# Kernel tuning notes

Hardware: AMD Instinct MI355X
Metric: run time of the kernel (lower is better)

Reference implementation:

```python
import jax, jax.numpy as jnp
import numpy as np

B, T, D = 16, 2048, 1024


def setup_inputs() -> dict:
    key = jax.random.key(0)
    ks = jax.random.split(key, 7)
    s = 1.0 / np.sqrt(D)  # nn.Linear default init bound
    u = lambda k, shape: jax.random.uniform(k, shape, jnp.float32, -s, s)
    return {
        "x": jax.random.normal(ks[0], (B, T, D), jnp.float32),
        "h0": jnp.zeros((B, D), jnp.float32),
        "W_in": u(ks[1], (2 * D, D)),
        "b_in": u(ks[2], (2 * D,)),
        "W_dt": u(ks[3], (D, D)),
        "b_dt": u(ks[4], (D,)),
        "W_out": u(ks[5], (D, D)),
        "b_out": u(ks[6], (D,)),
    }


def reference(x, h0, W_in, b_in, W_dt, b_dt, W_out, b_out):
    # in_proj then chunk: first half x_part, second half gate
    xz = jnp.einsum("btd,ed->bte", x, W_in) + b_in          # [B,T,2D]
    x_part, gate = jnp.split(xz, 2, axis=-1)                  # each [B,T,D]
    dt = jax.nn.sigmoid(jnp.einsum("btd,ed->bte", x_part, W_dt) + b_dt)  # [B,T,D]

    def step(h, inp):
        dt_t, xp_t = inp                                      # [B,D] each
        h = (1.0 - dt_t) * h + dt_t * xp_t                    # gated EMA update
        return h, h

    _, hs = jax.lax.scan(step, h0,
                         (jnp.swapaxes(dt, 0, 1), jnp.swapaxes(x_part, 0, 1)))
    hs = jnp.swapaxes(hs, 0, 1)                               # [B,T,D]
    y = jnp.einsum("btd,ed->bte", hs * jax.nn.sigmoid(gate), W_out) + b_out
    return y
```

## Files before the change

kernel.cpp:

```cpp
#include <hip/hip_runtime.h>
#include <hip/hip_bf16.h>
#include <cstdint>

typedef __attribute__((ext_vector_type(8))) short short8;
typedef __attribute__((ext_vector_type(4))) float f32x4;
typedef __attribute__((ext_vector_type(8))) unsigned short ushort8;

#define B_ 16
#define T_ 2048
#define D_ 1024
#define M_ (B_*T_)
#define NC 32
#define CL 64

static __device__ __forceinline__ float bf2f(unsigned short u) {
  unsigned int x = ((unsigned int)u) << 16;
  return __builtin_bit_cast(float, x);
}
static __device__ __forceinline__ unsigned short f2bf(float f) {
  unsigned int x = __builtin_bit_cast(unsigned int, f);
  unsigned int r = x + 0x7fffu + ((x >> 16) & 1u);
  return (unsigned short)(r >> 16);
}
static __device__ __forceinline__ float sigmoidf(float v) {
  return 1.f / (1.f + __expf(-v));
}

typedef const __attribute__((address_space(1))) unsigned int* gas1_t;
typedef __attribute__((address_space(3))) unsigned int* las3_t;
static __device__ __forceinline__ void async_copy16(const void* g, void* l) {
  __builtin_amdgcn_global_load_lds((gas1_t)g, (las3_t)l, 16, 0, 0);
}

#define VMCNT4 asm volatile("s_waitcnt vmcnt(4)" ::: "memory")
#define VMCNT2 asm volatile("s_waitcnt vmcnt(2)" ::: "memory")
#define VMCNT0 asm volatile("s_waitcnt vmcnt(0)" ::: "memory")
#define LGKM0  asm volatile("s_waitcnt lgkmcnt(0)" ::: "memory")
#define SBAR   __builtin_amdgcn_s_barrier()
#define SCHED0 __builtin_amdgcn_sched_barrier(0)

__global__ void cvt_all(const float* __restrict__ x,  unsigned short* __restrict__ xb,
                        const float* __restrict__ w1, unsigned short* __restrict__ o1,
                        const float* __restrict__ w2, unsigned short* __restrict__ o2,
                        const float* __restrict__ w3, unsigned short* __restrict__ o3) {
  long i = (long)blockIdx.x * blockDim.x + threadIdx.x;
  long stride = (long)gridDim.x * blockDim.x;
  for (; i < 4718592; i += stride) {
    const float* src; unsigned short* dst; long off;
    if (i < 4194304)      { src = x;  dst = xb; off = i; }
    else if (i < 4456448) { src = w1; dst = o1; off = i - 4194304; }
    else if (i < 4587520) { src = w2; dst = o2; off = i - 4456448; }
    else                  { src = w3; dst = o3; off = i - 4587520; }
    const float4* p = (const float4*)(src + off * 8);
    float4 a = p[0], b = p[1];
    ushort8 o;
    o[0] = f2bf(a.x); o[1] = f2bf(a.y); o[2] = f2bf(a.z); o[3] = f2bf(a.w);
    o[4] = f2bf(b.x); o[5] = f2bf(b.y); o[6] = f2bf(b.z); o[7] = f2bf(b.w);
    *(ushort8*)(dst + off * 8) = o;
  }
}

template<int EPI>
__global__ __launch_bounds__(512, 2) void gemm256(
    const unsigned short* __restrict__ A, long lda,
    const unsigned short* __restrict__ Bw,
    const float* __restrict__ bias,
    void* __restrict__ Cout, long ldc,
    int nbx)
{
  constexpr int KT = 16;
  __shared__ __align__(16) unsigned short lds[65536];

  const int tid = threadIdx.x;
  const int l  = tid & 63, w = tid >> 6;
  const int wm = w >> 2, wn = w & 3;
  const int fr = l & 15, g = l >> 4;
  const int t8 = tid >> 3;
  const int c8x = ((l & 7) ^ (l >> 3)) << 4;
  const int s0 = ((g ^ (fr & 7)) << 4);
  const int aoff  = wm * 8192 + fr * 128 + s0;
  const int aoff1 = aoff ^ 0x40;
  const int boff  = 65536 + wn * 4096 + fr * 128 + s0;
  const int boff1 = boff ^ 0x40;
  const int tB = (w >> 2) * 64 + (w & 3) * 8 + (l >> 3);

  const int nwg = gridDim.x;
  const int cpx = nwg >> 3;
  const int bid = blockIdx.x;
  const int swz = (bid & 7) * cpx + (bid >> 3);
  const long m0 = (long)(swz / nbx) * 256;
  const long n0 = (long)(swz % nbx) * 256;

  const char* Ab = (const char*)A;
  const char* Bb = (const char*)Bw;
  const long ldab = lda * 2;
  char* LB = (char*)lds;

  auto stA = [&](int kt, int h, int nb) {
    char* lb = LB + nb * 32768 + h * 16384 + w * 1024;
    long col = (long)kt * 128 + c8x;
    async_copy16(Ab + (m0 + h * 64 + t8) * ldab + col, lb);
    async_copy16(Ab + (m0 + 128 + h * 64 + t8) * ldab + col, lb + 8192);
  };
  auto stB = [&](int kt, int h, int nb) {
    char* lb = LB + 65536 + nb * 32768 + h * 16384 + w * 1024;
    long col = (long)kt * 128 + c8x;
    async_copy16(Bb + (n0 + tB + h * 32) * 2048 + col, lb);
    async_copy16(Bb + (n0 + tB + 128 + h * 32) * 2048 + col, lb + 8192);
  };

  f32x4 acc[8][4] = {};
  short8 af0[4][2], af1[4][2], bf0[2][2], bf1[2][2];

#define RD_A(DST, MH, CUR) do {                                                \
    const char* p0_ = LB + (CUR) * 32768 + (MH) * 16384 + aoff;                \
    const char* p1_ = LB + (CUR) * 32768 + (MH) * 16384 + aoff1;               \
    _Pragma("unroll") for (int mi = 0; mi < 4; ++mi) {                         \
      DST[mi][0] = *(const short8*)(p0_ + mi * 2048);                          \
      DST[mi][1] = *(const short8*)(p1_ + mi * 2048); }                        \
  } while (0)
#define RD_B(DST, NH, CUR) do {                                                \
    const char* p0_ = LB + (CUR) * 32768 + (NH) * 16384 + boff;                \
    const char* p1_ = LB + (CUR) * 32768 + (NH) * 16384 + boff1;               \
    _Pragma("unroll") for (int ni = 0; ni < 2; ++ni) {                         \
      DST[ni][0] = *(const short8*)(p0_ + ni * 2048);                          \
      DST[ni][1] = *(const short8*)(p1_ + ni * 2048); }                        \
  } while (0)
#define MM(AF, BF, MB, NB) do {                                                \
    __builtin_amdgcn_s_setprio(1);                                             \
    _Pragma("unroll") for (int mi = 0; mi < 4; ++mi)                           \
    _Pragma("unroll") for (int ni = 0; ni < 2; ++ni) {                         \
      acc[(MB)+mi][(NB)+ni] = __builtin_amdgcn_mfma_f32_16x16x32_bf16(         \
          AF[mi][0], BF[ni][0], acc[(MB)+mi][(NB)+ni], 0, 0, 0);               \
      acc[(MB)+mi][(NB)+ni] = __builtin_amdgcn_mfma_f32_16x16x32_bf16(         \
          AF[mi][1], BF[ni][1], acc[(MB)+mi][(NB)+ni], 0, 0, 0); }             \
    __builtin_amdgcn_s_setprio(0);                                             \
  } while (0)

  stA(0, 0, 0); stB(0, 0, 0); stA(0, 1, 0); stB(0, 1, 0);
  VMCNT0; SCHED0; SBAR;
  RD_A(af0, 0, 0); RD_B(bf0, 0, 0); SCHED0;

  for (int t = 0; t < KT; ++t) {
    const int cur = t & 1, nxt = cur ^ 1;
    const bool nl = (t + 1 < KT);
    RD_A(af1, 1, cur); SCHED0;
    if (nl) { stA(t + 1, 0, nxt); stB(t + 1, 0, nxt); } SCHED0;
    MM(af0, bf0, 0, 0);
    if (nl) { VMCNT4; } else { VMCNT0; }
    SCHED0; SBAR; SCHED0;
    RD_B(bf1, 1, cur); SCHED0;
    if (nl) { stA(t + 1, 1, nxt); stB(t + 1, 1, nxt); } SCHED0;
    MM(af1, bf0, 4, 0);
    SCHED0; SBAR; SCHED0;
    MM(af1, bf1, 4, 2);
    if (nl) { VMCNT4; }
    SCHED0; SBAR; SCHED0;
    MM(af0, bf1, 0, 2);
    SCHED0;
    if (nl) { RD_A(af0, 0, nxt); RD_B(bf0, 0, nxt); }
    SCHED0;
    if (nl) { VMCNT2; }
    SCHED0; SBAR; SCHED0;
  }
#undef RD_A
#undef RD_B
#undef MM

  __syncthreads();

  char* ep = LB + w * 16384;
  const int rq = l >> 4;
  if (EPI != 2) {
#pragma unroll
    for (int mi = 0; mi < 8; ++mi)
#pragma unroll
      for (int ni = 0; ni < 4; ++ni) {
        int cl = ni * 16 + fr;
        float bv = bias[n0 + wn * 64 + cl];
#pragma unroll
        for (int r = 0; r < 4; ++r) {
          float v = acc[mi][ni][r] + bv;
          if (EPI == 1) v = sigmoidf(v);
          int row = mi * 16 + rq * 4 + r;
          int byte = (row * 128 + cl * 2) ^ ((row & 7) << 4);
          *(unsigned short*)(ep + byte) = f2bf(v);
        }
      }
    LGKM0; SCHED0;
#pragma unroll
    for (int i = 0; i < 16; ++i) {
      int row = i * 8 + (l >> 3);
      int cb = (l & 7) * 16;
      int byte = (row * 128 + cb) ^ ((row & 7) << 4);
      short8 v = *(const short8*)(ep + byte);
      *(short8*)((unsigned short*)Cout + (m0 + wm * 128 + row) * ldc
                 + n0 + wn * 64 + (cb >> 1)) = v;
    }
  } else {
#pragma unroll
    for (int p = 0; p < 2; ++p) {
#pragma unroll
      for (int mi = 0; mi < 4; ++mi)
#pragma unroll
        for (int ni = 0; ni < 4; ++ni) {
          int cl = ni * 16 + fr;
          float bv = bias[n0 + wn * 64 + cl];
#pragma unroll
          for (int r = 0; r < 4; ++r) {
            float v = acc[p * 4 + mi][ni][r] + bv;
            int row = mi * 16 + rq * 4 + r;
            int byte = (row * 256 + cl * 4) ^ ((row & 7) << 4);
            *(float*)(ep + byte) = v;
          }
        }
      LGKM0; SCHED0;
#pragma unroll
      for (int i = 0; i < 16; ++i) {
        int row = i * 4 + (l >> 4);
        int cb = (l & 15) * 16;
        int byte = (row * 256 + cb) ^ ((row & 7) << 4);
        f32x4 v = *(const f32x4*)(ep + byte);
        *(f32x4*)((float*)Cout + (m0 + wm * 128 + p * 64 + row) * ldc
                  + n0 + wn * 64 + (cb >> 2)) = v;
      }
      LGKM0; SCHED0;
    }
  }
}

__global__ void scan_passA(const unsigned short* __restrict__ dtb,
                           const unsigned short* __restrict__ xz,
                           float* __restrict__ P, float* __restrict__ Hl)
{
  int idx = blockIdx.x * blockDim.x + threadIdx.x;
  int d8 = idx & 127;
  int c  = (idx >> 7) & 31;
  int b  = idx >> 12;
  int d0 = d8 * 8;
  long mbase = (long)b * T_ + (long)c * CL;
  float h[8] = {0,0,0,0,0,0,0,0};
  float p[8] = {1,1,1,1,1,1,1,1};
  for (int t = 0; t < CL; ++t) {
    long m = mbase + t;
    ushort8 dv = *(const ushort8*)(dtb + m * D_ + d0);
    ushort8 xv = *(const ushort8*)(xz + m * (2 * D_) + d0);
#pragma unroll
    for (int j = 0; j < 8; ++j) {
      float dt = bf2f(dv[j]);
      float xp = bf2f(xv[j]);
      float om = 1.f - dt;
      h[j] = om * h[j] + dt * xp;
      p[j] *= om;
    }
  }
  long pb = ((long)(b * NC + c)) * D_ + d0;
#pragma unroll
  for (int j = 0; j < 8; ++j) { P[pb + j] = p[j]; Hl[pb + j] = h[j]; }
}

__global__ void scan_passC(unsigned short* dts,
                           const unsigned short* __restrict__ xz,
                           const float* __restrict__ h0,
                           const float* __restrict__ P,
                           const float* __restrict__ Hl)
{
  int idx = blockIdx.x * blockDim.x + threadIdx.x;
  int d8 = idx & 127;
  int c  = (idx >> 7) & 31;
  int b  = idx >> 12;
  int d0 = d8 * 8;
  long mbase = (long)b * T_ + (long)c * CL;

  float h[8];
#pragma unroll
  for (int j = 0; j < 8; ++j) h[j] = h0[(long)b * D_ + d0 + j];

  for (int jc = 0; jc < c; ++jc) {
    long pb = ((long)(b * NC + jc)) * D_ + d0;
    float pj[8], hj[8];
    *(f32x4*)&pj[0] = *(const f32x4*)(P + pb);
    *(f32x4*)&pj[4] = *(const f32x4*)(P + pb + 4);
    *(f32x4*)&hj[0] = *(const f32x4*)(Hl + pb);
    *(f32x4*)&hj[4] = *(const f32x4*)(Hl + pb + 4);
#pragma unroll
    for (int j = 0; j < 8; ++j) h[j] = hj[j] + pj[j] * h[j];
  }

  for (int t = 0; t < CL; ++t) {
    long m = mbase + t;
    ushort8 dv = *(const ushort8*)(dts + m * D_ + d0);
    ushort8 xv = *(const ushort8*)(xz + m * (2 * D_) + d0);
    ushort8 gv = *(const ushort8*)(xz + m * (2 * D_) + D_ + d0);
    ushort8 ov;
#pragma unroll
    for (int j = 0; j < 8; ++j) {
      float dt = bf2f(dv[j]);
      float xp = bf2f(xv[j]);
      h[j] = (1.f - dt) * h[j] + dt * xp;
      float gt = bf2f(gv[j]);
      ov[j] = f2bf(h[j] * sigmoidf(gt));
    }
    *(ushort8*)(dts + m * D_ + d0) = ov;
  }
}

extern "C" void kernel_launch(void* const* d_in, const int* in_sizes, int n_in,
                              void* d_out, int out_size, void* d_ws, size_t ws_size,
                              hipStream_t stream) {
  const float* x     = (const float*)d_in[0];
  const float* h0    = (const float*)d_in[1];
  const float* W_in  = (const float*)d_in[2];
  const float* b_in  = (const float*)d_in[3];
  const float* W_dt  = (const float*)d_in[4];
  const float* b_dt  = (const float*)d_in[5];
  const float* W_out = (const float*)d_in[6];
  const float* b_out = (const float*)d_in[7];
  float* out = (float*)d_out;

  char* ws = (char*)d_ws;
  const size_t OFF_XB    = 0;
  const size_t OFF_WIN   = 67108864;
  const size_t OFF_WDT   = 71303168;
  const size_t OFF_WOUT  = 73400320;
  const size_t OFF_XZ    = 75497472;
  const size_t OFF_DTS   = 209715200;
  const size_t OFF_P     = 276824064;
  const size_t OFF_HL    = 278921216;
  const size_t NEEDED    = 281018368;
  if (ws_size < NEEDED) return;

  unsigned short* xb    = (unsigned short*)(ws + OFF_XB);
  unsigned short* wbin  = (unsigned short*)(ws + OFF_WIN);
  unsigned short* wbdt  = (unsigned short*)(ws + OFF_WDT);
  unsigned short* wbout = (unsigned short*)(ws + OFF_WOUT);
  unsigned short* xz    = (unsigned short*)(ws + OFF_XZ);
  unsigned short* dts   = (unsigned short*)(ws + OFF_DTS);
  float* P  = (float*)(ws + OFF_P);
  float* Hl = (float*)(ws + OFF_HL);

  cvt_all<<<2048, 256, 0, stream>>>(x, xb, W_in, wbin, W_dt, wbdt, W_out, wbout);

  gemm256<0><<<(M_/256)*(2*D_/256), 512, 0, stream>>>(xb, D_, wbin, b_in, xz, 2*D_, 2*D_/256);
  gemm256<1><<<(M_/256)*(D_/256), 512, 0, stream>>>(xz, 2*D_, wbdt, b_dt, dts, D_, D_/256);
  scan_passA<<<256, 256, 0, stream>>>(dts, xz, P, Hl);
  scan_passC<<<256, 256, 0, stream>>>(dts, xz, h0, P, Hl);
  gemm256<2><<<(M_/256)*(D_/256), 512, 0, stream>>>(dts, D_, wbout, b_out, out, D_, D_/256);
}
```

Baseline: 443.9 us.

## Switch GEMM inner tiles from 16x16x32 to 32x32x16 bf16 MFMA

Replaces the 16x16x32 MFMA tiling in the 256x256 GEMM with 32x32x16 MFMA instructions. LDS fragment reads, the swizzle offsets, the accumulator layout (f32x16) and the epilogue row mapping are all reworked to match. The larger MFMA shape issues fewer instructions and reads fewer LDS fragments per FLOP, which should cut LDS traffic and issue overhead. In exchange it changes register pressure, and the new swizzle pattern may introduce bank conflicts.

```diff
diff --git a/kernel.cpp b/kernel.cpp
--- a/kernel.cpp
+++ b/kernel.cpp
@@ -4,6 +4,7 @@
 
 typedef __attribute__((ext_vector_type(8))) short short8;
 typedef __attribute__((ext_vector_type(4))) float f32x4;
+typedef __attribute__((ext_vector_type(16))) float f32x16;
 typedef __attribute__((ext_vector_type(8))) unsigned short ushort8;
 
 #define B_ 16
@@ -74,14 +75,11 @@
   const int tid = threadIdx.x;
   const int l  = tid & 63, w = tid >> 6;
   const int wm = w >> 2, wn = w & 3;
-  const int fr = l & 15, g = l >> 4;
   const int t8 = tid >> 3;
   const int c8x = ((l & 7) ^ (l >> 3)) << 4;
-  const int s0 = ((g ^ (fr & 7)) << 4);
-  const int aoff  = wm * 8192 + fr * 128 + s0;
-  const int aoff1 = aoff ^ 0x40;
-  const int boff  = 65536 + wn * 4096 + fr * 128 + s0;
-  const int boff1 = boff ^ 0x40;
+  const int kb  = (((l >> 5) ^ (l & 7)) << 4);
+  const int a32off = wm * 8192 + (l & 31) * 128;
+  const int b32off = 65536 + wn * 4096 + (l & 31) * 128;
   const int tB = (w >> 2) * 64 + (w & 3) * 8 + (l >> 3);
 
   const int nwg = gridDim.x;
@@ -109,31 +107,26 @@
     async_copy16(Bb + (n0 + tB + 128 + h * 32) * 2048 + col, lb + 8192);
   };
 
-  f32x4 acc[8][4] = {};
-  short8 af0[4][2], af1[4][2], bf0[2][2], bf1[2][2];
+  f32x16 acc[4][2] = {};
+  short8 af0[2][4], af1[2][4], bf0[4], bf1[4];
 
 #define RD_A(DST, MH, CUR) do {                                                \
-    const char* p0_ = LB + (CUR) * 32768 + (MH) * 16384 + aoff;                \
-    const char* p1_ = LB + (CUR) * 32768 + (MH) * 16384 + aoff1;               \
-    _Pragma("unroll") for (int mi = 0; mi < 4; ++mi) {                         \
-      DST[mi][0] = *(const short8*)(p0_ + mi * 2048);                          \
-      DST[mi][1] = *(const short8*)(p1_ + mi * 2048); }                        \
+    const char* p_ = LB + (CUR) * 32768 + (MH) * 16384 + a32off;               \
+    _Pragma("unroll") for (int mi = 0; mi < 2; ++mi)                           \
+    _Pragma("unroll") for (int kk = 0; kk < 4; ++kk)                           \
+      DST[mi][kk] = *(const short8*)(p_ + mi * 4096 + ((kk * 32) ^ kb));       \
   } while (0)
 #define RD_B(DST, NH, CUR) do {                                                \
-    const char* p0_ = LB + (CUR) * 32768 + (NH) * 16384 + boff;                \
-    const char* p1_ = LB + (CUR) * 32768 + (NH) * 16384 + boff1;               \
-    _Pragma("unroll") for (int ni = 0; ni < 2; ++ni) {                         \
-      DST[ni][0] = *(const short8*)(p0_ + ni * 2048);                          \
-      DST[ni][1] = *(const short8*)(p1_ + ni * 2048); }                        \
+    const char* p_ = LB + (CUR) * 32768 + (NH) * 16384 + b32off;               \
+    _Pragma("unroll") for (int kk = 0; kk < 4; ++kk)                           \
+      DST[kk] = *(const short8*)(p_ + ((kk * 32) ^ kb));                       \
   } while (0)
-#define MM(AF, BF, MB, NB) do {                                                \
+#define MM(AF, BF, MH, NH) do {                                                \
     __builtin_amdgcn_s_setprio(1);                                             \
-    _Pragma("unroll") for (int mi = 0; mi < 4; ++mi)                           \
-    _Pragma("unroll") for (int ni = 0; ni < 2; ++ni) {                         \
-      acc[(MB)+mi][(NB)+ni] = __builtin_amdgcn_mfma_f32_16x16x32_bf16(         \
-          AF[mi][0], BF[ni][0], acc[(MB)+mi][(NB)+ni], 0, 0, 0);               \
-      acc[(MB)+mi][(NB)+ni] = __builtin_amdgcn_mfma_f32_16x16x32_bf16(         \
-          AF[mi][1], BF[ni][1], acc[(MB)+mi][(NB)+ni], 0, 0, 0); }             \
+    _Pragma("unroll") for (int kk = 0; kk < 4; ++kk)                           \
+    _Pragma("unroll") for (int mi = 0; mi < 2; ++mi)                           \
+      acc[(MH)*2+mi][NH] = __builtin_amdgcn_mfma_f32_32x32x16_bf16(            \
+          AF[mi][kk], BF[kk], acc[(MH)*2+mi][NH], 0, 0, 0);                    \
     __builtin_amdgcn_s_setprio(0);                                             \
   } while (0)
 
@@ -151,12 +144,12 @@
     SCHED0; SBAR; SCHED0;
     RD_B(bf1, 1, cur); SCHED0;
     if (nl) { stA(t + 1, 1, nxt); stB(t + 1, 1, nxt); } SCHED0;
-    MM(af1, bf0, 4, 0);
+    MM(af1, bf0, 1, 0);
     SCHED0; SBAR; SCHED0;
-    MM(af1, bf1, 4, 2);
+    MM(af1, bf1, 1, 1);
     if (nl) { VMCNT4; }
     SCHED0; SBAR; SCHED0;
-    MM(af0, bf1, 0, 2);
+    MM(af0, bf1, 0, 1);
     SCHED0;
     if (nl) { RD_A(af0, 0, nxt); RD_B(bf0, 0, nxt); }
     SCHED0;
@@ -170,19 +163,18 @@
   __syncthreads();
 
   char* ep = LB + w * 16384;
-  const int rq = l >> 4;
   if (EPI != 2) {
 #pragma unroll
-    for (int mi = 0; mi < 8; ++mi)
-#pragma unroll
-      for (int ni = 0; ni < 4; ++ni) {
-        int cl = ni * 16 + fr;
+    for (int ar = 0; ar < 4; ++ar)
+#pragma unroll
+      for (int ni = 0; ni < 2; ++ni) {
+        int cl = ni * 32 + (l & 31);
         float bv = bias[n0 + wn * 64 + cl];
 #pragma unroll
-        for (int r = 0; r < 4; ++r) {
-          float v = acc[mi][ni][r] + bv;
+        for (int r = 0; r < 16; ++r) {
+          float v = acc[ar][ni][r] + bv;
           if (EPI == 1) v = sigmoidf(v);
-          int row = mi * 16 + rq * 4 + r;
+          int row = ar * 32 + (r & 3) + 8 * (r >> 2) + 4 * (l >> 5);
           int byte = (row * 128 + cl * 2) ^ ((row & 7) << 4);
           *(unsigned short*)(ep + byte) = f2bf(v);
         }
@@ -201,19 +193,21 @@
 #pragma unroll
     for (int p = 0; p < 2; ++p) {
 #pragma unroll
-      for (int mi = 0; mi < 4; ++mi)
-#pragma unroll
-        for (int ni = 0; ni < 4; ++ni) {
-          int cl = ni * 16 + fr;
+      for (int ai = 0; ai < 2; ++ai) {
+        int ar = p * 2 + ai;
+#pragma unroll
+        for (int ni = 0; ni < 2; ++ni) {
+          int cl = ni * 32 + (l & 31);
           float bv = bias[n0 + wn * 64 + cl];
 #pragma unroll
-          for (int r = 0; r < 4; ++r) {
-            float v = acc[p * 4 + mi][ni][r] + bv;
-            int row = mi * 16 + rq * 4 + r;
-            int byte = (row * 256 + cl * 4) ^ ((row & 7) << 4);
+          for (int r = 0; r < 16; ++r) {
+            float v = acc[ar][ni][r] + bv;
+            int row64 = ai * 32 + (r & 3) + 8 * (r >> 2) + 4 * (l >> 5);
+            int byte = (row64 * 256 + cl * 4) ^ ((row64 & 7) << 4);
             *(float*)(ep + byte) = v;
           }
         }
+      }
       LGKM0; SCHED0;
 #pragma unroll
       for (int i = 0; i < 16; ++i) {
```

New measurement: 485.7 us. +9.4%, slower.

## Restructure GEMM main loop schedule to single A fragment buffer with finer waits

Applied to the files above, without the earlier changes.

Reworks the software pipeline of the bf16 MFMA GEMM main loop. It drops the double-buffered A register fragments, reorders the quadrant MMAs and LDS reads, and replaces the full vmcnt(0) drain with partial vmcnt waits so staged global loads overlap more with compute. Lower register pressure may raise occupancy or scheduling freedom. The extra barriers and lgkmcnt waits inside each iteration expose LDS latency that the prefetched fragments used to hide, and the vmcnt counts must match the load order exactly to stay correct.

```diff
diff --git a/kernel.cpp b/kernel.cpp
--- a/kernel.cpp
+++ b/kernel.cpp
@@ -32,6 +32,8 @@
   __builtin_amdgcn_global_load_lds((gas1_t)g, (las3_t)l, 16, 0, 0);
 }
 
+#define VMCNT8 asm volatile("s_waitcnt vmcnt(8)" ::: "memory")
+#define VMCNT6 asm volatile("s_waitcnt vmcnt(6)" ::: "memory")
 #define VMCNT4 asm volatile("s_waitcnt vmcnt(4)" ::: "memory")
 #define VMCNT2 asm volatile("s_waitcnt vmcnt(2)" ::: "memory")
 #define VMCNT0 asm volatile("s_waitcnt vmcnt(0)" ::: "memory")
@@ -110,7 +112,7 @@
   };
 
   f32x4 acc[8][4] = {};
-  short8 af0[4][2], af1[4][2], bf0[2][2], bf1[2][2];
+  short8 af[4][2], bf0[2][2], bf1[2][2];
 
 #define RD_A(DST, MH, CUR) do {                                                \
     const char* p0_ = LB + (CUR) * 32768 + (MH) * 16384 + aoff;                \
@@ -137,30 +139,29 @@
     __builtin_amdgcn_s_setprio(0);                                             \
   } while (0)
 
-  stA(0, 0, 0); stB(0, 0, 0); stA(0, 1, 0); stB(0, 1, 0);
-  VMCNT0; SCHED0; SBAR;
-  RD_A(af0, 0, 0); RD_B(bf0, 0, 0); SCHED0;
+  stA(0, 0, 0); stB(0, 0, 0); stB(0, 1, 0); stA(0, 1, 0);
+  VMCNT4; SCHED0; SBAR;
 
   for (int t = 0; t < KT; ++t) {
     const int cur = t & 1, nxt = cur ^ 1;
     const bool nl = (t + 1 < KT);
-    RD_A(af1, 1, cur); SCHED0;
+    RD_A(af, 0, cur); RD_B(bf0, 0, cur); SCHED0;
     if (nl) { stA(t + 1, 0, nxt); stB(t + 1, 0, nxt); } SCHED0;
-    MM(af0, bf0, 0, 0);
-    if (nl) { VMCNT4; } else { VMCNT0; }
+    SBAR; LGKM0; SCHED0;
+    MM(af, bf0, 0, 0);
+    if (nl) { VMCNT6; } else { VMCNT2; }
     SCHED0; SBAR; SCHED0;
     RD_B(bf1, 1, cur); SCHED0;
-    if (nl) { stA(t + 1, 1, nxt); stB(t + 1, 1, nxt); } SCHED0;
-    MM(af1, bf0, 4, 0);
+    if (nl) { stB(t + 1, 1, nxt); stA(t + 1, 1, nxt); } SCHED0;
+    SBAR; LGKM0; SCHED0;
+    MM(af, bf1, 0, 2);
+    if (nl) { VMCNT8; } else { VMCNT0; }
     SCHED0; SBAR; SCHED0;
-    MM(af1, bf1, 4, 2);
+    RD_A(af, 1, cur); SCHED0;
+    SBAR; LGKM0; SCHED0;
+    MM(af, bf0, 4, 0);
+    MM(af, bf1, 4, 2);
     if (nl) { VMCNT4; }
-    SCHED0; SBAR; SCHED0;
-    MM(af0, bf1, 0, 2);
-    SCHED0;
-    if (nl) { RD_A(af0, 0, nxt); RD_B(bf0, 0, nxt); }
-    SCHED0;
-    if (nl) { VMCNT2; }
     SCHED0; SBAR; SCHED0;
   }
 #undef RD_A
```

Result: no change. 439.8 us (-0.9%).
